# Kernel optimization log

Measured on AMD Instinct MI355X. Metric: run time of the kernel, lower is better.

Reference implementation:

```python
import jax, jax.numpy as jnp
import numpy as np

NUM_CLASSES = 20
LAMBDA_COORD = 5.0
BATCH_SIZE = 512
ANCHORS = [[1.3221, 1.73145], [3.19275, 4.00944], [5.05587, 8.09892],
           [9.47112, 4.84053], [11.2364, 10.0071]]


def setup_inputs() -> dict:
    key = jax.random.key(0)
    k1, k2 = jax.random.split(key)
    prediction = jax.random.normal(k1, (512, 125, 13, 13), dtype=jnp.float32)
    # target: conf in [0,1), xy in [0,1), wh positive -> uniform is a valid fill
    target = jax.random.uniform(k2, (512, 13, 13, 125), dtype=jnp.float32)
    anchors = jnp.asarray(ANCHORS, dtype=jnp.float32)
    return {"prediction": prediction, "target": target, "anchors": anchors}


def _pairwise_iou(a, b):
    """a, b: [B, HW, A, 4] center-format (x, y, w, h).
    Returns pairwise IoU [B, HW, A, A] between a-anchors and b-boxes."""
    a = a[..., :, None, :]  # [B,HW,A,1,4]
    b = b[..., None, :, :]  # [B,HW,1,A,4]
    ax1, ay1 = a[..., 0] - a[..., 2] * 0.5, a[..., 1] - a[..., 3] * 0.5
    ax2, ay2 = a[..., 0] + a[..., 2] * 0.5, a[..., 1] + a[..., 3] * 0.5
    bx1, by1 = b[..., 0] - b[..., 2] * 0.5, b[..., 1] - b[..., 3] * 0.5
    bx2, by2 = b[..., 0] + b[..., 2] * 0.5, b[..., 1] + b[..., 3] * 0.5
    iw = jnp.clip(jnp.minimum(ax2, bx2) - jnp.maximum(ax1, bx1), 0.0)
    ih = jnp.clip(jnp.minimum(ay2, by2) - jnp.maximum(ay1, by1), 0.0)
    inter = iw * ih
    area_a = (ax2 - ax1) * (ay2 - ay1)
    area_b = (bx2 - bx1) * (by2 - by1)
    return inter / (area_a + area_b - inter + 1e-10)


def reference(prediction, target, anchors):
    bsize, _, h, w = prediction.shape
    A = anchors.shape[0]
    C = 5 + NUM_CLASSES
    out = jnp.transpose(prediction, (0, 2, 3, 1)).reshape(bsize, h * w * A, C)
    tgt = target.reshape(bsize, h * w * A, C)

    # decode predictions
    pred_xy = jax.nn.sigmoid(out[..., 21:23])
    pred_wh = jnp.exp(out[..., 23:25])
    pred_box = jnp.concatenate([pred_xy, pred_wh], axis=-1).reshape(bsize, h * w, A, 4)

    gt_box = jnp.concatenate([tgt[..., 21:23], tgt[..., 23:25]], axis=-1)
    gt_box = gt_box.reshape(bsize, h * w, A, 4)
    gt_conf = tgt[..., 20].reshape(bsize, h * w, A, 1)

    # anchor boxes: predicted centers with prior (anchor) width/height
    anc_wh = jnp.broadcast_to(anchors[None, None], (bsize, h * w, A, 2))
    anc_box = jnp.concatenate([pred_box[..., :2], anc_wh], axis=-1)

    iou = _pairwise_iou(anc_box, gt_box)            # [B, HW, A, A]
    anchor_idx = jnp.argmax(iou, axis=-1)           # [B, HW, A]

    # torch fancy-index write mask[:, :, anchor_idx, :] = gt_conf[:, :, anchor_idx, :]
    # assigns gt_conf at every anchor slot whose index appears anywhere in anchor_idx;
    # uncovered slots stay zero.
    covered = jnp.zeros((A,), dtype=bool).at[anchor_idx.reshape(-1)].set(True)
    mask = jnp.where(covered[None, None, :, None], gt_conf, 0.0)

    diff = pred_box * mask - gt_box * mask
    box_loss = (LAMBDA_COORD / BATCH_SIZE) * jnp.sum(diff * diff)
    return box_loss
```

## Files before the change

### kernel.cpp

```cpp
#include <hip/hip_runtime.h>
#include <math.h>

#define NB 512
#define HW 169
#define NA 5
#define NCH 125
#define BLOCK 256
#define NBLOCKS ((NB * HW) / BLOCK)
#define REC 8

__global__ __launch_bounds__(BLOCK, 2) void yolo_loss_main(
    const float* __restrict__ P,
    const float* __restrict__ T,
    const float* __restrict__ ANC,
    float* __restrict__ brec)
{
    int idx = blockIdx.x * BLOCK + threadIdx.x;
    int b  = idx / HW;
    int hw = idx - b * HW;

    const float* Pb = P + (size_t)b * NCH * HW + hw;
    const float* Tb = T + ((size_t)b * HW + hw) * NCH;

    float rx[NA], ry[NA], rw[NA], rh[NA];
    float gx[NA], gy[NA], gw_[NA], gh[NA], gc[NA];
#pragma unroll
    for (int a = 0; a < NA; ++a) {
        int c0 = a * 25;
        rx[a] = Pb[(c0 + 21) * HW];
        ry[a] = Pb[(c0 + 22) * HW];
        rw[a] = Pb[(c0 + 23) * HW];
        rh[a] = Pb[(c0 + 24) * HW];
    }
#pragma unroll
    for (int a = 0; a < NA; ++a) {
        int c0 = a * 25;
        gc[a]  = Tb[c0 + 20];
        gx[a]  = Tb[c0 + 21];
        gy[a]  = Tb[c0 + 22];
        gw_[a] = Tb[c0 + 23];
        gh[a]  = Tb[c0 + 24];
    }

    float px[NA], py[NA], pw[NA], ph[NA];
#pragma unroll
    for (int a = 0; a < NA; ++a) {
        px[a] = 1.0f / (1.0f + expf(-rx[a]));
        py[a] = 1.0f / (1.0f + expf(-ry[a]));
        pw[a] = expf(rw[a]);
        ph[a] = expf(rh[a]);
    }

    float contrib[NA];
    int cmask = 0;
#pragma unroll
    for (int i = 0; i < NA; ++i) {
        float aw = ANC[2 * i], ah = ANC[2 * i + 1];
        float ax1 = px[i] - aw * 0.5f, ax2 = px[i] + aw * 0.5f;
        float ay1 = py[i] - ah * 0.5f, ay2 = py[i] + ah * 0.5f;
        float area_a = (ax2 - ax1) * (ay2 - ay1);
        float best = -1.0f; int bestj = 0;
#pragma unroll
        for (int j = 0; j < NA; ++j) {
            float bx1 = gx[j] - gw_[j] * 0.5f, bx2 = gx[j] + gw_[j] * 0.5f;
            float by1 = gy[j] - gh[j] * 0.5f, by2 = gy[j] + gh[j] * 0.5f;
            float iw = fmaxf(fminf(ax2, bx2) - fmaxf(ax1, bx1), 0.0f);
            float ih = fmaxf(fminf(ay2, by2) - fmaxf(ay1, by1), 0.0f);
            float inter = iw * ih;
            float area_b = (bx2 - bx1) * (by2 - by1);
            float iou = inter / (area_a + area_b - inter + 1e-10f);
            if (iou > best) { best = iou; bestj = j; }
        }
        cmask |= (1 << bestj);
        float dx = px[i] - gx[i], dy = py[i] - gy[i];
        float dw = pw[i] - gw_[i], dh = ph[i] - gh[i];
        contrib[i] = gc[i] * gc[i] * (dx * dx + dy * dy + dw * dw + dh * dh);
    }

    __shared__ float sred[4][NA];
    __shared__ int smask[4];
    int lane = threadIdx.x & 63, wid = threadIdx.x >> 6;

#pragma unroll
    for (int i = 0; i < NA; ++i) {
        float v = contrib[i];
        for (int off = 32; off; off >>= 1) v += __shfl_down(v, off, 64);
        if (lane == 0) sred[wid][i] = v;
    }
    for (int off = 32; off; off >>= 1) cmask |= __shfl_down(cmask, off, 64);
    if (lane == 0) smask[wid] = cmask;
    __syncthreads();

    if (threadIdx.x == 0) {
        int m = smask[0] | smask[1] | smask[2] | smask[3];
        float* r = brec + blockIdx.x * REC;
#pragma unroll
        for (int i = 0; i < NA; ++i)
            r[i] = sred[0][i] + sred[1][i] + sred[2][i] + sred[3][i];
        ((int*)r)[5] = m;
    }
}

__global__ void yolo_loss_final(const float* __restrict__ brec,
                                float* __restrict__ out)
{
    int lane = threadIdx.x;
    double s[NA] = {0, 0, 0, 0, 0};
    int m = 0;
    for (int e = lane; e < NBLOCKS; e += 64) {
        const float* r = brec + e * REC;
#pragma unroll
        for (int i = 0; i < NA; ++i) s[i] += (double)r[i];
        m |= ((const int*)r)[5];
    }
#pragma unroll
    for (int i = 0; i < NA; ++i)
        for (int off = 32; off; off >>= 1) s[i] += __shfl_down(s[i], off, 64);
    for (int off = 32; off; off >>= 1) m |= __shfl_down(m, off, 64);

    if (lane == 0) {
        double tot = 0.0;
#pragma unroll
        for (int i = 0; i < NA; ++i)
            if ((m >> i) & 1) tot += s[i];
        out[0] = (float)((5.0 / 512.0) * tot);
    }
}

extern "C" void kernel_launch(void* const* d_in, const int* in_sizes, int n_in,
                              void* d_out, int out_size, void* d_ws, size_t ws_size,
                              hipStream_t stream) {
    const float* P   = (const float*)d_in[0];
    const float* T   = (const float*)d_in[1];
    const float* ANC = (const float*)d_in[2];
    float* out = (float*)d_out;

    float* brec = (float*)d_ws;

    yolo_loss_main<<<NBLOCKS, BLOCK, 0, stream>>>(P, T, ANC, brec);
    yolo_loss_final<<<1, 64, 0, stream>>>(brec, out);
}
```

Before: 20.17 us.

## Stage target slab through LDS with coalesced float4 loads

```diff
diff --git a/kernel.cpp b/kernel.cpp
--- a/kernel.cpp
+++ b/kernel.cpp
@@ -8,6 +8,7 @@
 #define BLOCK 256
 #define NBLOCKS ((NB * HW) / BLOCK)
 #define REC 8
+#define SLAB_F4 ((BLOCK * NCH) / 4)
 
 __global__ __launch_bounds__(BLOCK, 2) void yolo_loss_main(
     const float* __restrict__ P,
@@ -15,15 +16,15 @@
     const float* __restrict__ ANC,
     float* __restrict__ brec)
 {
-    int idx = blockIdx.x * BLOCK + threadIdx.x;
-    int b  = idx / HW;
-    int hw = idx - b * HW;
+    __shared__ float sT[BLOCK][25];
+
+    int t = threadIdx.x;
+    int gcell = blockIdx.x * BLOCK + t;
+    int b  = gcell / HW;
+    int hw = gcell - b * HW;
 
     const float* Pb = P + (size_t)b * NCH * HW + hw;
-    const float* Tb = T + ((size_t)b * HW + hw) * NCH;
-
     float rx[NA], ry[NA], rw[NA], rh[NA];
-    float gx[NA], gy[NA], gw_[NA], gh[NA], gc[NA];
 #pragma unroll
     for (int a = 0; a < NA; ++a) {
         int c0 = a * 25;
@@ -32,19 +33,37 @@
         rw[a] = Pb[(c0 + 23) * HW];
         rh[a] = Pb[(c0 + 24) * HW];
     }
+
+    const float4* T4 = (const float4*)T + (size_t)blockIdx.x * SLAB_F4;
+#pragma unroll 4
+    for (int k = 0; k < 32; ++k) {
+        int li = t + k * BLOCK;
+        if (li < SLAB_F4) {
+            float4 v = T4[li];
+            float vv[4] = {v.x, v.y, v.z, v.w};
+            int Lf = li * 4;
+#pragma unroll
+            for (int i = 0; i < 4; ++i) {
+                int c = Lf + i;
+                int cell = c / 125;
+                int chan = c - cell * 125;
+                int a = chan / 25;
+                int r = chan - a * 25;
+                if (r >= 20) sT[cell][a * 5 + (r - 20)] = vv[i];
+            }
+        }
+    }
+    __syncthreads();
+
+    float px[NA], py[NA], pw[NA], ph[NA];
+    float gx[NA], gy[NA], gw_[NA], gh[NA], gc[NA];
 #pragma unroll
     for (int a = 0; a < NA; ++a) {
-        int c0 = a * 25;
-        gc[a]  = Tb[c0 + 20];
-        gx[a]  = Tb[c0 + 21];
-        gy[a]  = Tb[c0 + 22];
-        gw_[a] = Tb[c0 + 23];
-        gh[a]  = Tb[c0 + 24];
-    }
-
-    float px[NA], py[NA], pw[NA], ph[NA];
-#pragma unroll
-    for (int a = 0; a < NA; ++a) {
+        gc[a]  = sT[t][a * 5 + 0];
+        gx[a]  = sT[t][a * 5 + 1];
+        gy[a]  = sT[t][a * 5 + 2];
+        gw_[a] = sT[t][a * 5 + 3];
+        gh[a]  = sT[t][a * 5 + 4];
         px[a] = 1.0f / (1.0f + expf(-rx[a]));
         py[a] = 1.0f / (1.0f + expf(-ry[a]));
         pw[a] = expf(rw[a]);
@@ -79,7 +98,7 @@
 
     __shared__ float sred[4][NA];
     __shared__ int smask[4];
-    int lane = threadIdx.x & 63, wid = threadIdx.x >> 6;
+    int lane = t & 63, wid = t >> 6;
 
 #pragma unroll
     for (int i = 0; i < NA; ++i) {
@@ -91,13 +110,15 @@
     if (lane == 0) smask[wid] = cmask;
     __syncthreads();
 
-    if (threadIdx.x == 0) {
+    if (t == 0) {
         int m = smask[0] | smask[1] | smask[2] | smask[3];
         float* r = brec + blockIdx.x * REC;
 #pragma unroll
         for (int i = 0; i < NA; ++i)
             r[i] = sred[0][i] + sred[1][i] + sred[2][i] + sred[3][i];
         ((int*)r)[5] = m;
+        ((int*)r)[6] = 0;
+        ((int*)r)[7] = 0;
     }
 }
 
@@ -105,13 +126,16 @@
                                 float* __restrict__ out)
 {
     int lane = threadIdx.x;
+    const float4* r4 = (const float4*)brec;
     double s[NA] = {0, 0, 0, 0, 0};
     int m = 0;
     for (int e = lane; e < NBLOCKS; e += 64) {
-        const float* r = brec + e * REC;
-#pragma unroll
-        for (int i = 0; i < NA; ++i) s[i] += (double)r[i];
-        m |= ((const int*)r)[5];
+        float4 lo = r4[e * 2];
+        float4 hi = r4[e * 2 + 1];
+        s[0] += (double)lo.x; s[1] += (double)lo.y;
+        s[2] += (double)lo.z; s[3] += (double)lo.w;
+        s[4] += (double)hi.x;
+        m |= __float_as_int(hi.y);
     }
 #pragma unroll
     for (int i = 0; i < NA; ++i)
```

Measured after the change: 33.69 us. 1.67x slower.
